# Kernel tuning notes

Measured on AMD Instinct MI355X. Metric: run time of the kernel, lower is better.

## Reference

```python
import jax, jax.numpy as jnp
import numpy as np
import math

EPS = 1e-8
MIN_RADIUS = 0.1
SINH_MAX = math.asinh(2.0 ** 15)
CURV = 1.0                     # exp(clamp(log(1.0), log(0.1), log(10)))
IMAGE_ALPHA = 0.25             # exp(clamp(log(1/4), max=0))
TEXT_ALPHA = 1.0 / 0.6         # exp(log(1/0.6)), frozen
LOGIT_SCALE = 1.0 / 0.07       # exp(clamp(log(1/0.07), max=4.6052))
ENTAIL_WEIGHT = 0.2


def exp_map0(x, curv):
    # MERU exponential map at the Lorentz-model origin (space components only).
    rc = jnp.sqrt(curv) * jnp.linalg.norm(x, axis=-1, keepdims=True)
    sinh_in = jnp.clip(rc, EPS, SINH_MAX)
    return jnp.sinh(sinh_in) * x / jnp.maximum(rc, EPS)


def pairwise_dist(x, y, curv):
    # x: (B,H,W,D) image feats on hyperboloid; y: (C,D) text protos. -> (B,H,W,C)
    x_time = jnp.sqrt(1.0 / curv + jnp.sum(x * x, axis=-1))   # (B,H,W)
    y_time = jnp.sqrt(1.0 / curv + jnp.sum(y * y, axis=-1))   # (C,)
    inner = jnp.einsum('bhwd,cd->bhwc', x, y) - x_time[..., None] * y_time
    c_xyl = -curv * inner
    return jnp.arccosh(jnp.maximum(c_xyl, 1.0 + EPS)) / jnp.sqrt(curv)


def oxy_angle(x, y, curv):
    # Exterior angle at x between origin->x and x->y geodesics. x,y: (...,D) -> (...,)
    x_time = jnp.sqrt(1.0 / curv + jnp.sum(x * x, axis=-1))
    y_time = jnp.sqrt(1.0 / curv + jnp.sum(y * y, axis=-1))
    c_xyl = curv * (jnp.sum(x * y, axis=-1) - x_time * y_time)
    acos_num = y_time + c_xyl * x_time
    acos_den = jnp.linalg.norm(x, axis=-1) * jnp.sqrt(jnp.maximum(c_xyl * c_xyl - 1.0, 0.0))
    acos_in = acos_num / (acos_den + EPS)
    return jnp.arccos(jnp.clip(acos_in, -1.0 + EPS, 1.0 - EPS))


def half_aperture(x, curv):
    asin_in = 2.0 * MIN_RADIUS / (jnp.linalg.norm(x, axis=-1) * jnp.sqrt(curv) + EPS)
    return jnp.arcsin(jnp.clip(asin_in, -1.0 + EPS, 1.0 - EPS))


def _forward(feats, text_protos, labels, mask):
    curv = jnp.float32(CURV)
    img = exp_map0(feats * IMAGE_ALPHA, curv)          # (B,H,W,D)
    txt = exp_map0(text_protos * TEXT_ALPHA, curv)     # (C,D)

    dist = pairwise_dist(img, txt, curv)               # (B,H,W,C)
    proto = txt[labels]                                # (B,H,W,D) gather by GT class
    angle = oxy_angle(proto, img, curv)                # (B,H,W)
    aperture = half_aperture(proto, curv)              # (B,H,W)

    logits = LOGIT_SCALE * (-dist)                     # scale * image_logits
    logp = jax.nn.log_softmax(logits, axis=-1)
    nll = -jnp.take_along_axis(logp, labels[..., None], axis=-1)[..., 0]

    valid = (~mask).astype(jnp.float32)                # mask==1 means ignore
    n_valid = jnp.maximum(jnp.sum(valid), 1.0)
    sup_loss = jnp.sum(nll * valid) / n_valid

    ent = jnp.maximum(angle - aperture, 0.0)
    entail_loss = jnp.sum(ent * valid) / n_valid

    return sup_loss + ENTAIL_WEIGHT * entail_loss


def setup_inputs() -> dict:
    key = jax.random.key(0)
    k1, k2, k3, k4 = jax.random.split(key, 4)
    B, H, W, D, C = 2, 512, 512, 64, 151
    feats = jax.random.normal(k1, (B, H, W, D), dtype=jnp.float32)
    text_protos = jax.random.normal(k2, (C, D), dtype=jnp.float32)
    labels = jax.random.randint(k3, (B, H, W), 0, C, dtype=jnp.int32)
    mask = jax.random.randint(k4, (B, H, W), 0, 2, dtype=jnp.int32).astype(bool)
    return {"feats": feats, "text_protos": text_protos, "labels": labels, "mask": mask}


def reference(feats, text_protos, labels, mask):
    return _forward(feats, text_protos, labels, mask)
```

## Files before the change

kernel.cpp:

```cpp
#include <hip/hip_runtime.h>
#include <math.h>

#define EPSF 1e-8f
#define SINH_MAXF 11.090354888959125f
#define IMAGE_ALPHA 0.25f
#define TEXT_ALPHA (1.0f/0.6f)
#define LOGIT_SCALE (1.0f/0.07f)
#define LN2F 0.6931471805599453f
#define SLN (LOGIT_SCALE*LN2F)
#define ENTAIL_WEIGHT 0.2f
#define NCLS 151
#define NPAD 160
#define DIM 64
#define NBLK 4096

#define LMIN_OFF 8
#define YT_OFF 16
#define XN_OFF (YT_OFF + NPAD)
#define AP_OFF (XN_OFF + NPAD)
#define BT_OFF 512
#define BLK_OFF (BT_OFF + NPAD*DIM/2)

typedef __attribute__((ext_vector_type(8))) short bf16x8;
typedef __attribute__((ext_vector_type(4))) float f32x4;

__device__ inline unsigned short f2bf(float f) {
    unsigned int u = __float_as_uint(f);
    return (unsigned short)((u + 0x7FFFu + ((u >> 16) & 1u)) >> 16);
}
__device__ inline unsigned int pack_bf_trunc(float hi, float lo) {
    return __builtin_amdgcn_perm(__float_as_uint(hi), __float_as_uint(lo), 0x07060302u);
}
__device__ inline float sel4(const float* a, int i) {
    return i == 0 ? a[0] : i == 1 ? a[1] : i == 2 ? a[2] : a[3];
}
__device__ inline int isel4(const int* a, int i) {
    return i == 0 ? a[0] : i == 1 ? a[1] : i == 2 ? a[2] : a[3];
}

__global__ __launch_bounds__(256) void proto_kernel(const float* __restrict__ protos,
                                                    float* __restrict__ ws) {
    int tid = threadIdx.x, w = tid >> 6, l = tid & 63;
    unsigned short* bt = (unsigned short*)(ws + BT_OFF);
    __shared__ float sYT[NPAD];
    for (int c = w; c < NPAD; c += 4) {
        int t = c >> 4, cn = c & 15;
        int half = l >> 5, g = (l >> 3) & 3, j = l & 7;
        int sidx = (t * 128 + half * 64 + g * 16 + cn) * 8 + j;
        float yt_c;
        if (c < NCLS) {
            float v = protos[c * DIM + l] * TEXT_ALPHA;
            float n2 = v * v;
            #pragma unroll
            for (int m = 32; m >= 1; m >>= 1) n2 += __shfl_xor(n2, m, 64);
            float rc = __builtin_amdgcn_sqrtf(n2);
            float rr = fminf(fmaxf(rc, EPSF), SINH_MAXF);
            float e = __expf(rr);
            float sh = 0.5f * (e - __builtin_amdgcn_rcpf(e));
            float sc = sh * __builtin_amdgcn_rcpf(fmaxf(rc, EPSF));
            bt[sidx] = f2bf(sc * v);
            float xn = sc * rc;
            yt_c = __builtin_amdgcn_sqrtf(fmaf(xn, xn, 1.f));
            if (l == 0) {
                ws[YT_OFF + c] = yt_c;
                ws[XN_OFF + c] = xn;
                float ai = fminf(fmaxf(0.2f / (xn + EPSF), -1.f + EPSF), 1.f - EPSF);
                ws[AP_OFF + c] = asinf(ai);
            }
        } else {
            bt[sidx] = 0;
            yt_c = 2e18f;
            if (l == 0) { ws[YT_OFF + c] = 2e18f; ws[XN_OFF + c] = 1.f; ws[AP_OFF + c] = 0.f; }
        }
        if (l == 0) sYT[c] = yt_c;
    }
    __syncthreads();
    if (tid < 64) {
        float m = 1e30f;
        for (int c = tid; c < NCLS; c += 64) m = fminf(m, sYT[c]);
        #pragma unroll
        for (int k = 32; k >= 1; k >>= 1) m = fminf(m, __shfl_xor(m, k, 64));
        if (tid == 0) ws[LMIN_OFF] = __log2f(2.f * m);
    }
}

struct PixA { bf16x8 q0, q1; float xt, Q; };

__device__ inline PixA stage_pixel(const float4* fp, float lmin2) {
    float4 f0 = fp[0], f1 = fp[1], f2 = fp[8], f3 = fp[9];
    float n2r = f0.x*f0.x + f0.y*f0.y + f0.z*f0.z + f0.w*f0.w
              + f1.x*f1.x + f1.y*f1.y + f1.z*f1.z + f1.w*f1.w
              + f2.x*f2.x + f2.y*f2.y + f2.z*f2.z + f2.w*f2.w
              + f3.x*f3.x + f3.y*f3.y + f3.z*f3.z + f3.w*f3.w;
    n2r += __shfl_xor(n2r, 16, 64);
    n2r += __shfl_xor(n2r, 32, 64);
    float rc = IMAGE_ALPHA * __builtin_amdgcn_sqrtf(n2r);
    float rr = fminf(fmaxf(rc, EPSF), SINH_MAXF);
    float e = __expf(rr);
    float sh = 0.5f * (e - __builtin_amdgcn_rcpf(e));
    float sc = sh * __builtin_amdgcn_rcpf(fmaxf(rc, EPSF));
    float xn = sc * rc;
    float k = sc * IMAGE_ALPHA;
    PixA r;
    r.xt = __builtin_amdgcn_sqrtf(fmaf(xn, xn, 1.f));
    r.Q = SLN * (lmin2 - __log2f(r.xt + xn)) - SLN;
    unsigned int* q0u = (unsigned int*)&r.q0;
    unsigned int* q1u = (unsigned int*)&r.q1;
    q0u[0] = pack_bf_trunc(k*f0.y, k*f0.x);
    q0u[1] = pack_bf_trunc(k*f0.w, k*f0.z);
    q0u[2] = pack_bf_trunc(k*f1.y, k*f1.x);
    q0u[3] = pack_bf_trunc(k*f1.w, k*f1.z);
    q1u[0] = pack_bf_trunc(k*f2.y, k*f2.x);
    q1u[1] = pack_bf_trunc(k*f2.w, k*f2.z);
    q1u[2] = pack_bf_trunc(k*f3.y, k*f3.x);
    q1u[3] = pack_bf_trunc(k*f3.w, k*f3.z);
    return r;
}

__global__ __launch_bounds__(256) void main_kernel(
    const float* __restrict__ feats, const int* __restrict__ labels,
    const unsigned char* __restrict__ mask, const float* __restrict__ wsro,
    float4* __restrict__ blkout)
{
    __shared__ uint4 sBT[1280];
    __shared__ float sYT[NPAD];
    int tid = threadIdx.x;
    const uint4* btg = (const uint4*)(wsro + BT_OFF);
    #pragma unroll
    for (int k = 0; k < 5; k++) sBT[tid + k * 256] = btg[tid + k * 256];
    if (tid < NPAD) sYT[tid] = wsro[YT_OFF + tid];
    __syncthreads();

    int wid = tid >> 6, lane = tid & 63;
    int cn = lane & 15, g = lane >> 4;
    int wavebase = (blockIdx.x * 4 + wid) * 32;
    int pix0 = wavebase + cn, pix1 = pix0 + 16;
    float lmin2 = wsro[LMIN_OFF];

    PixA A0 = stage_pixel((const float4*)(feats + (size_t)pix0 * DIM + g * 8), lmin2);
    PixA A1 = stage_pixel((const float4*)(feats + (size_t)pix1 * DIM + g * 8), lmin2);
    int lab0 = labels[pix0], lab1 = labels[pix1];

    float xtr0[4], Q0[4], xtr1[4], Q1[4];
    int lr0[4], lr1[4];
    #pragma unroll
    for (int r = 0; r < 4; r++) {
        int src = g * 4 + r;
        xtr0[r] = __shfl(A0.xt, src, 64); Q0[r] = __shfl(A0.Q, src, 64);
        lr0[r]  = __shfl(lab0, src, 64);
        xtr1[r] = __shfl(A1.xt, src, 64); Q1[r] = __shfl(A1.Q, src, 64);
        lr1[r]  = __shfl(lab1, src, 64);
    }

    float ss0[4] = {0,0,0,0}, ss1[4] = {0,0,0,0};
    float sv0[4] = {0,0,0,0}, sv1[4] = {0,0,0,0};

    #pragma unroll 2
    for (int t = 0; t < 10; t++) {
        uint4 u0 = sBT[t * 128 + lane];
        uint4 u1 = sBT[t * 128 + 64 + lane];
        bf16x8 bq0 = __builtin_bit_cast(bf16x8, u0);
        bf16x8 bq1 = __builtin_bit_cast(bf16x8, u1);
        float yt = sYT[t * 16 + cn];
        int cls = t * 16 + cn;
        f32x4 d0 = {0,0,0,0}, d1 = {0,0,0,0};
        d0 = __builtin_amdgcn_mfma_f32_16x16x32_bf16(A0.q0, bq0, d0, 0, 0, 0);
        d0 = __builtin_amdgcn_mfma_f32_16x16x32_bf16(A0.q1, bq1, d0, 0, 0, 0);
        d1 = __builtin_amdgcn_mfma_f32_16x16x32_bf16(A1.q0, bq0, d1, 0, 0, 0);
        d1 = __builtin_amdgcn_mfma_f32_16x16x32_bf16(A1.q1, bq1, d1, 0, 0, 0);
        #pragma unroll
        for (int r = 0; r < 4; r++) {
            float c0 = fmaf(xtr0[r], yt, -d0[r]);
            if (lr0[r] == cls) sv0[r] = c0;
            ss0[r] += __expf(fmaf(-SLN, __log2f(c0), Q0[r]));
            float c1 = fmaf(xtr1[r], yt, -d1[r]);
            if (lr1[r] == cls) sv1[r] = c1;
            ss1[r] += __expf(fmaf(-SLN, __log2f(c1), Q1[r]));
        }
    }

    int gbase = lane & 48;
    float cx0[4], cx1[4];
    #pragma unroll
    for (int r = 0; r < 4; r++) {
        cx0[r] = __shfl(sv0[r], gbase + (lr0[r] & 15), 64);
        cx1[r] = __shfl(sv1[r], gbase + (lr1[r] & 15), 64);
    }
    #pragma unroll
    for (int k = 1; k < 16; k <<= 1) {
        #pragma unroll
        for (int r = 0; r < 4; r++) {
            ss0[r] += __shfl_xor(ss0[r], k, 64);
            ss1[r] += __shfl_xor(ss1[r], k, 64);
        }
    }

    float v_nll = 0.f, v_ent = 0.f, valid = 0.f;
    if (cn < 4) {
        #pragma unroll
        for (int tile = 0; tile < 2; tile++) {
            float T   = tile ? sel4(ss1, cn) : sel4(ss0, cn);
            float cxl = tile ? sel4(cx1, cn) : sel4(cx0, cn);
            float xts = tile ? sel4(xtr1, cn) : sel4(xtr0, cn);
            float Q   = tile ? sel4(Q1, cn) : sel4(Q0, cn);
            int lb    = tile ? isel4(lr1, cn) : isel4(lr0, cn);
            int pr = wavebase + g * 4 + cn + tile * 16;
            float nll = __logf(T) - Q + SLN * __log2f(cxl);
            float pt = wsro[YT_OFF + lb], pn = wsro[XN_OFF + lb], ap = wsro[AP_OFF + lb];
            float num = fmaf(-cxl, pt, xts);
            float den = pn * __builtin_amdgcn_sqrtf(fmaxf(fmaf(cxl, cxl, -1.f), 0.f));
            float ain = num * __builtin_amdgcn_rcpf(den + EPSF);
            ain = fminf(fmaxf(ain, -1.f + EPSF), 1.f - EPSF);
            float ax = fabsf(ain);
            float p = fmaf(fmaf(fmaf(-0.0187293f, ax, 0.0742610f), ax, -0.2121144f),
                           ax, 1.5707288f);
            float rr = __builtin_amdgcn_sqrtf(1.f - ax) * p;
            float ac = ain < 0.f ? 3.14159265358979f - rr : rr;
            float ent = fmaxf(ac - ap, 0.f);
            float vl = mask[pr] ? 0.f : 1.f;
            v_nll += nll * vl; v_ent += ent * vl; valid += vl;
        }
    }

    #pragma unroll
    for (int o = 32; o >= 1; o >>= 1) {
        v_nll += __shfl_down(v_nll, o, 64);
        v_ent += __shfl_down(v_ent, o, 64);
        valid += __shfl_down(valid, o, 64);
    }
    __shared__ float red[3][4];
    if (lane == 0) { red[0][wid] = v_nll; red[1][wid] = v_ent; red[2][wid] = valid; }
    __syncthreads();
    if (tid == 0) {
        float a = 0.f, b = 0.f, c = 0.f;
        #pragma unroll
        for (int w = 0; w < 4; w++) { a += red[0][w]; b += red[1][w]; c += red[2][w]; }
        blkout[blockIdx.x] = make_float4(a, b, c, 0.f);
    }
}

__global__ __launch_bounds__(1024) void reduce_kernel(const float4* __restrict__ blk,
                                                      float* __restrict__ out) {
    float a = 0.f, b = 0.f, c = 0.f;
    for (int i = threadIdx.x; i < NBLK; i += 1024) {
        float4 v = blk[i];
        a += v.x; b += v.y; c += v.z;
    }
    #pragma unroll
    for (int o = 32; o >= 1; o >>= 1) {
        a += __shfl_down(a, o, 64);
        b += __shfl_down(b, o, 64);
        c += __shfl_down(c, o, 64);
    }
    __shared__ float red[3][16];
    int wid = threadIdx.x >> 6, lane = threadIdx.x & 63;
    if (lane == 0) { red[0][wid] = a; red[1][wid] = b; red[2][wid] = c; }
    __syncthreads();
    if (threadIdx.x == 0) {
        float A = 0.f, B = 0.f, C = 0.f;
        #pragma unroll
        for (int w = 0; w < 16; w++) { A += red[0][w]; B += red[1][w]; C += red[2][w]; }
        float n = fmaxf(C, 1.f);
        out[0] = A / n + ENTAIL_WEIGHT * (B / n);
    }
}

extern "C" void kernel_launch(void* const* d_in, const int* in_sizes, int n_in,
                              void* d_out, int out_size, void* d_ws, size_t ws_size,
                              hipStream_t stream) {
    const float* feats  = (const float*)d_in[0];
    const float* protos = (const float*)d_in[1];
    const int* labels   = (const int*)d_in[2];
    const unsigned char* mask = (const unsigned char*)d_in[3];
    float* ws = (float*)d_ws;

    proto_kernel<<<1, 256, 0, stream>>>(protos, ws);

    int npix = in_sizes[2];
    int nblk = npix / 128;
    main_kernel<<<nblk, 256, 0, stream>>>(feats, labels, mask, ws,
                                          (float4*)(ws + BLK_OFF));
    reduce_kernel<<<1, 1024, 0, stream>>>((const float4*)(ws + BLK_OFF), (float*)d_out);
}
```

Before: 237.9 us.

## Halve grid with two pixel chunks per block and fuse final reduction via ticket

Result: slower. 369.0 us (+55.1%).

```diff
diff --git a/kernel.cpp b/kernel.cpp
--- a/kernel.cpp
+++ b/kernel.cpp
@@ -12,8 +12,11 @@
 #define NCLS 151
 #define NPAD 160
 #define DIM 64
-#define NBLK 4096
-
+#define NBLK 2048
+#define NCHUNK 2
+#define CHUNK_STRIDE (NBLK*4*32)
+
+#define CNT_OFF 0
 #define LMIN_OFF 8
 #define YT_OFF 16
 #define XN_OFF (YT_OFF + NPAD)
@@ -120,7 +123,7 @@
 __global__ __launch_bounds__(256) void main_kernel(
     const float* __restrict__ feats, const int* __restrict__ labels,
     const unsigned char* __restrict__ mask, const float* __restrict__ wsro,
-    float4* __restrict__ blkout)
+    float4* __restrict__ blkout, int* __restrict__ ticket, float* __restrict__ out)
 {
     __shared__ uint4 sBT[1280];
     __shared__ float sYT[NPAD];
@@ -133,92 +136,100 @@
 
     int wid = tid >> 6, lane = tid & 63;
     int cn = lane & 15, g = lane >> 4;
-    int wavebase = (blockIdx.x * 4 + wid) * 32;
-    int pix0 = wavebase + cn, pix1 = pix0 + 16;
     float lmin2 = wsro[LMIN_OFF];
 
-    PixA A0 = stage_pixel((const float4*)(feats + (size_t)pix0 * DIM + g * 8), lmin2);
-    PixA A1 = stage_pixel((const float4*)(feats + (size_t)pix1 * DIM + g * 8), lmin2);
-    int lab0 = labels[pix0], lab1 = labels[pix1];
-
-    float xtr0[4], Q0[4], xtr1[4], Q1[4];
-    int lr0[4], lr1[4];
+    float ytv[10];
     #pragma unroll
-    for (int r = 0; r < 4; r++) {
-        int src = g * 4 + r;
-        xtr0[r] = __shfl(A0.xt, src, 64); Q0[r] = __shfl(A0.Q, src, 64);
-        lr0[r]  = __shfl(lab0, src, 64);
-        xtr1[r] = __shfl(A1.xt, src, 64); Q1[r] = __shfl(A1.Q, src, 64);
-        lr1[r]  = __shfl(lab1, src, 64);
-    }
-
-    float ss0[4] = {0,0,0,0}, ss1[4] = {0,0,0,0};
-    float sv0[4] = {0,0,0,0}, sv1[4] = {0,0,0,0};
-
-    #pragma unroll 2
-    for (int t = 0; t < 10; t++) {
-        uint4 u0 = sBT[t * 128 + lane];
-        uint4 u1 = sBT[t * 128 + 64 + lane];
-        bf16x8 bq0 = __builtin_bit_cast(bf16x8, u0);
-        bf16x8 bq1 = __builtin_bit_cast(bf16x8, u1);
-        float yt = sYT[t * 16 + cn];
-        int cls = t * 16 + cn;
-        f32x4 d0 = {0,0,0,0}, d1 = {0,0,0,0};
-        d0 = __builtin_amdgcn_mfma_f32_16x16x32_bf16(A0.q0, bq0, d0, 0, 0, 0);
-        d0 = __builtin_amdgcn_mfma_f32_16x16x32_bf16(A0.q1, bq1, d0, 0, 0, 0);
-        d1 = __builtin_amdgcn_mfma_f32_16x16x32_bf16(A1.q0, bq0, d1, 0, 0, 0);
-        d1 = __builtin_amdgcn_mfma_f32_16x16x32_bf16(A1.q1, bq1, d1, 0, 0, 0);
+    for (int t = 0; t < 10; t++) ytv[t] = sYT[t * 16 + cn];
+
+    float v_nll = 0.f, v_ent = 0.f, valid = 0.f;
+
+    for (int chunk = 0; chunk < NCHUNK; chunk++) {
+        int wavebase = (blockIdx.x * 4 + wid) * 32 + chunk * CHUNK_STRIDE;
+        int pix0 = wavebase + cn, pix1 = pix0 + 16;
+
+        PixA A0 = stage_pixel((const float4*)(feats + (size_t)pix0 * DIM + g * 8), lmin2);
+        PixA A1 = stage_pixel((const float4*)(feats + (size_t)pix1 * DIM + g * 8), lmin2);
+        int lab0 = labels[pix0], lab1 = labels[pix1];
+
+        float xtr0[4], Q0[4], xtr1[4], Q1[4];
+        int lr0[4], lr1[4];
         #pragma unroll
         for (int r = 0; r < 4; r++) {
-            float c0 = fmaf(xtr0[r], yt, -d0[r]);
-            if (lr0[r] == cls) sv0[r] = c0;
-            ss0[r] += __expf(fmaf(-SLN, __log2f(c0), Q0[r]));
-            float c1 = fmaf(xtr1[r], yt, -d1[r]);
-            if (lr1[r] == cls) sv1[r] = c1;
-            ss1[r] += __expf(fmaf(-SLN, __log2f(c1), Q1[r]));
-        }
-    }
-
-    int gbase = lane & 48;
-    float cx0[4], cx1[4];
-    #pragma unroll
-    for (int r = 0; r < 4; r++) {
-        cx0[r] = __shfl(sv0[r], gbase + (lr0[r] & 15), 64);
-        cx1[r] = __shfl(sv1[r], gbase + (lr1[r] & 15), 64);
-    }
-    #pragma unroll
-    for (int k = 1; k < 16; k <<= 1) {
+            int src = g * 4 + r;
+            xtr0[r] = __shfl(A0.xt, src, 64); Q0[r] = __shfl(A0.Q, src, 64);
+            lr0[r]  = __shfl(lab0, src, 64);
+            xtr1[r] = __shfl(A1.xt, src, 64); Q1[r] = __shfl(A1.Q, src, 64);
+            lr1[r]  = __shfl(lab1, src, 64);
+        }
+
+        float ss0[4] = {0,0,0,0}, ss1[4] = {0,0,0,0};
+        float sv0[4] = {0,0,0,0}, sv1[4] = {0,0,0,0};
+
+        #pragma unroll 2
+        for (int t = 0; t < 10; t++) {
+            uint4 u0 = sBT[t * 128 + lane];
+            uint4 u1 = sBT[t * 128 + 64 + lane];
+            bf16x8 bq0 = __builtin_bit_cast(bf16x8, u0);
+            bf16x8 bq1 = __builtin_bit_cast(bf16x8, u1);
+            float yt = ytv[t];
+            int cls = t * 16 + cn;
+            f32x4 d0 = {0,0,0,0}, d1 = {0,0,0,0};
+            d0 = __builtin_amdgcn_mfma_f32_16x16x32_bf16(A0.q0, bq0, d0, 0, 0, 0);
+            d0 = __builtin_amdgcn_mfma_f32_16x16x32_bf16(A0.q1, bq1, d0, 0, 0, 0);
+            d1 = __builtin_amdgcn_mfma_f32_16x16x32_bf16(A1.q0, bq0, d1, 0, 0, 0);
+            d1 = __builtin_amdgcn_mfma_f32_16x16x32_bf16(A1.q1, bq1, d1, 0, 0, 0);
+            #pragma unroll
+            for (int r = 0; r < 4; r++) {
+                float c0 = fmaf(xtr0[r], yt, -d0[r]);
+                if (lr0[r] == cls) sv0[r] = c0;
+                ss0[r] += __expf(fmaf(-SLN, __log2f(c0), Q0[r]));
+                float c1 = fmaf(xtr1[r], yt, -d1[r]);
+                if (lr1[r] == cls) sv1[r] = c1;
+                ss1[r] += __expf(fmaf(-SLN, __log2f(c1), Q1[r]));
+            }
+        }
+
+        int gbase = lane & 48;
+        float cx0[4], cx1[4];
         #pragma unroll
         for (int r = 0; r < 4; r++) {
-            ss0[r] += __shfl_xor(ss0[r], k, 64);
-            ss1[r] += __shfl_xor(ss1[r], k, 64);
-        }
-    }
-
-    float v_nll = 0.f, v_ent = 0.f, valid = 0.f;
-    if (cn < 4) {
-        #pragma unroll
-        for (int tile = 0; tile < 2; tile++) {
-            float T   = tile ? sel4(ss1, cn) : sel4(ss0, cn);
-            float cxl = tile ? sel4(cx1, cn) : sel4(cx0, cn);
-            float xts = tile ? sel4(xtr1, cn) : sel4(xtr0, cn);
-            float Q   = tile ? sel4(Q1, cn) : sel4(Q0, cn);
-            int lb    = tile ? isel4(lr1, cn) : isel4(lr0, cn);
-            int pr = wavebase + g * 4 + cn + tile * 16;
-            float nll = __logf(T) - Q + SLN * __log2f(cxl);
-            float pt = wsro[YT_OFF + lb], pn = wsro[XN_OFF + lb], ap = wsro[AP_OFF + lb];
-            float num = fmaf(-cxl, pt, xts);
-            float den = pn * __builtin_amdgcn_sqrtf(fmaxf(fmaf(cxl, cxl, -1.f), 0.f));
-            float ain = num * __builtin_amdgcn_rcpf(den + EPSF);
-            ain = fminf(fmaxf(ain, -1.f + EPSF), 1.f - EPSF);
-            float ax = fabsf(ain);
-            float p = fmaf(fmaf(fmaf(-0.0187293f, ax, 0.0742610f), ax, -0.2121144f),
-                           ax, 1.5707288f);
-            float rr = __builtin_amdgcn_sqrtf(1.f - ax) * p;
-            float ac = ain < 0.f ? 3.14159265358979f - rr : rr;
-            float ent = fmaxf(ac - ap, 0.f);
-            float vl = mask[pr] ? 0.f : 1.f;
-            v_nll += nll * vl; v_ent += ent * vl; valid += vl;
+            cx0[r] = __shfl(sv0[r], gbase + (lr0[r] & 15), 64);
+            cx1[r] = __shfl(sv1[r], gbase + (lr1[r] & 15), 64);
+        }
+        #pragma unroll
+        for (int k = 1; k < 16; k <<= 1) {
+            #pragma unroll
+            for (int r = 0; r < 4; r++) {
+                ss0[r] += __shfl_xor(ss0[r], k, 64);
+                ss1[r] += __shfl_xor(ss1[r], k, 64);
+            }
+        }
+
+        if (cn < 4) {
+            #pragma unroll
+            for (int tile = 0; tile < 2; tile++) {
+                float T   = tile ? sel4(ss1, cn) : sel4(ss0, cn);
+                float cxl = tile ? sel4(cx1, cn) : sel4(cx0, cn);
+                float xts = tile ? sel4(xtr1, cn) : sel4(xtr0, cn);
+                float Q   = tile ? sel4(Q1, cn) : sel4(Q0, cn);
+                int lb    = tile ? isel4(lr1, cn) : isel4(lr0, cn);
+                int pr = wavebase + g * 4 + cn + tile * 16;
+                float nll = __logf(T) - Q + SLN * __log2f(cxl);
+                float pt = wsro[YT_OFF + lb], pn = wsro[XN_OFF + lb], ap = wsro[AP_OFF + lb];
+                float num = fmaf(-cxl, pt, xts);
+                float den = pn * __builtin_amdgcn_sqrtf(fmaxf(fmaf(cxl, cxl, -1.f), 0.f));
+                float ain = num * __builtin_amdgcn_rcpf(den + EPSF);
+                ain = fminf(fmaxf(ain, -1.f + EPSF), 1.f - EPSF);
+                float ax = fabsf(ain);
+                float p = fmaf(fmaf(fmaf(-0.0187293f, ax, 0.0742610f), ax, -0.2121144f),
+                               ax, 1.5707288f);
+                float rr = __builtin_amdgcn_sqrtf(1.f - ax) * p;
+                float ac = ain < 0.f ? 3.14159265358979f - rr : rr;
+                float ent = fmaxf(ac - ap, 0.f);
+                float vl = mask[pr] ? 0.f : 1.f;
+                v_nll += nll * vl; v_ent += ent * vl; valid += vl;
+            }
         }
     }
 
@@ -231,37 +242,40 @@
     __shared__ float red[3][4];
     if (lane == 0) { red[0][wid] = v_nll; red[1][wid] = v_ent; red[2][wid] = valid; }
     __syncthreads();
+    __shared__ int amLast;
     if (tid == 0) {
         float a = 0.f, b = 0.f, c = 0.f;
         #pragma unroll
         for (int w = 0; w < 4; w++) { a += red[0][w]; b += red[1][w]; c += red[2][w]; }
         blkout[blockIdx.x] = make_float4(a, b, c, 0.f);
-    }
-}
-
-__global__ __launch_bounds__(1024) void reduce_kernel(const float4* __restrict__ blk,
-                                                      float* __restrict__ out) {
-    float a = 0.f, b = 0.f, c = 0.f;
-    for (int i = threadIdx.x; i < NBLK; i += 1024) {
-        float4 v = blk[i];
-        a += v.x; b += v.y; c += v.z;
-    }
-    #pragma unroll
-    for (int o = 32; o >= 1; o >>= 1) {
-        a += __shfl_down(a, o, 64);
-        b += __shfl_down(b, o, 64);
-        c += __shfl_down(c, o, 64);
-    }
-    __shared__ float red[3][16];
-    int wid = threadIdx.x >> 6, lane = threadIdx.x & 63;
-    if (lane == 0) { red[0][wid] = a; red[1][wid] = b; red[2][wid] = c; }
-    __syncthreads();
-    if (threadIdx.x == 0) {
-        float A = 0.f, B = 0.f, C = 0.f;
-        #pragma unroll
-        for (int w = 0; w < 16; w++) { A += red[0][w]; B += red[1][w]; C += red[2][w]; }
-        float n = fmaxf(C, 1.f);
-        out[0] = A / n + ENTAIL_WEIGHT * (B / n);
+        __threadfence();
+        int t = atomicAdd(ticket, 1);
+        amLast = (t == NBLK - 1);
+    }
+    __syncthreads();
+
+    if (amLast) {
+        __threadfence();
+        const volatile float* bf = (const volatile float*)blkout;
+        float a = 0.f, b = 0.f, c = 0.f;
+        for (int i = tid; i < NBLK; i += 256) {
+            a += bf[i * 4 + 0]; b += bf[i * 4 + 1]; c += bf[i * 4 + 2];
+        }
+        #pragma unroll
+        for (int o = 32; o >= 1; o >>= 1) {
+            a += __shfl_down(a, o, 64);
+            b += __shfl_down(b, o, 64);
+            c += __shfl_down(c, o, 64);
+        }
+        if (lane == 0) { red[0][wid] = a; red[1][wid] = b; red[2][wid] = c; }
+        __syncthreads();
+        if (tid == 0) {
+            float A = 0.f, B = 0.f, C = 0.f;
+            #pragma unroll
+            for (int w = 0; w < 4; w++) { A += red[0][w]; B += red[1][w]; C += red[2][w]; }
+            float n = fmaxf(C, 1.f);
+            out[0] = A / n + ENTAIL_WEIGHT * (B / n);
+        }
     }
 }
 
@@ -274,11 +288,9 @@
     const unsigned char* mask = (const unsigned char*)d_in[3];
     float* ws = (float*)d_ws;
 
+    hipMemsetAsync(ws, 0, 16, stream);
     proto_kernel<<<1, 256, 0, stream>>>(protos, ws);
-
-    int npix = in_sizes[2];
-    int nblk = npix / 128;
-    main_kernel<<<nblk, 256, 0, stream>>>(feats, labels, mask, ws,
-                                          (float4*)(ws + BLK_OFF));
-    reduce_kernel<<<1, 1024, 0, stream>>>((const float4*)(ws + BLK_OFF), (float*)d_out);
-}
+    main_kernel<<<NBLK, 256, 0, stream>>>(feats, labels, mask, ws,
+                                          (float4*)(ws + BLK_OFF),
+                                          (int*)(ws + CNT_OFF), (float*)d_out);
+}
```
